# Performance work log

Measured on AMD Instinct MI355X. Metric: run time of the kernel, lower is better.

Reference implementation:

```python
import jax, jax.numpy as jnp
import numpy as np

DIM = 1024
HEADS = 16
HEAD_DIM = DIM // HEADS


def setup_inputs() -> dict:
    key = jax.random.key(0)
    ks = jax.random.split(key, 5)
    B, N = 4, 2048
    x = jax.random.normal(ks[0], (B, N, DIM), dtype=jnp.float32)
    # nn.Linear default init scale ~ 1/sqrt(fan_in)
    s = 1.0 / np.sqrt(DIM)
    W_qkv = jax.random.uniform(ks[1], (DIM, 3 * DIM), minval=-s, maxval=s, dtype=jnp.float32)
    b_qkv = jax.random.uniform(ks[2], (3 * DIM,), minval=-s, maxval=s, dtype=jnp.float32)
    W_proj = jax.random.uniform(ks[3], (DIM, DIM), minval=-s, maxval=s, dtype=jnp.float32)
    b_proj = jax.random.uniform(ks[4], (DIM,), minval=-s, maxval=s, dtype=jnp.float32)
    return {"x": x, "W_qkv": W_qkv, "b_qkv": b_qkv, "W_proj": W_proj, "b_proj": b_proj}


def reference(x, W_qkv, b_qkv, W_proj, b_proj):
    B, N, C = x.shape
    qkv = x @ W_qkv + b_qkv                      # [B, N, 3C]
    qkv = qkv.reshape(B, N, 3, HEADS, HEAD_DIM)
    q = jnp.transpose(qkv[:, :, 0], (0, 2, 1, 3))  # [B, H, N, D]
    k = jnp.transpose(qkv[:, :, 1], (0, 2, 1, 3))
    v = jnp.transpose(qkv[:, :, 2], (0, 2, 1, 3))
    scale = 1.0 / np.sqrt(HEAD_DIM)
    scores = jnp.einsum('bhqd,bhkd->bhqk', q, k) * scale  # [B, H, N, N]
    attn = jax.nn.softmax(scores, axis=-1)
    out = jnp.einsum('bhqk,bhkd->bhqd', attn, v)           # [B, H, N, D]
    out = jnp.transpose(out, (0, 2, 1, 3)).reshape(B, N, C)
    return out @ W_proj + b_proj
```

## Files before the change

kernel.cpp:

```cpp
#include <hip/hip_runtime.h>

typedef __attribute__((ext_vector_type(2)))  float  f32x2;
typedef __attribute__((ext_vector_type(4)))  float  f32x4;
typedef __attribute__((ext_vector_type(16))) float  f32x16;
typedef __attribute__((ext_vector_type(8)))  short  short8;
typedef __attribute__((ext_vector_type(4)))  unsigned int u32x4;
typedef __attribute__((ext_vector_type(2)))  unsigned int uint2v;

#define MFMA16 __builtin_amdgcn_mfma_f32_16x16x32_bf16
#define MFMA32 __builtin_amdgcn_mfma_f32_32x32x16_bf16

static __device__ __forceinline__ unsigned short f2bf(float f){
  union { float f; unsigned u; } v; v.f = f;
  unsigned r = v.u + 0x7fffu + ((v.u >> 16) & 1u);
  return (unsigned short)(r >> 16);
}

static __device__ __forceinline__ unsigned cvtpk(float a, float b){
  unsigned r;
  asm("v_cvt_pk_bf16_f32 %0, %1, %2" : "=v"(r) : "v"(a), "v"(b));
  return r;
}

static __device__ __forceinline__ void plswap(unsigned &a, unsigned &b){
  asm("v_permlane32_swap_b32 %0, %1" : "+v"(a), "+v"(b));
}

static __device__ __forceinline__ float max3f(float a, float b, float c){
  return fmaxf(fmaxf(a, b), c);
}

typedef __attribute__((address_space(1))) void gvoid_t;
typedef __attribute__((address_space(3))) void lvoid_t;

static __device__ __forceinline__ void gll16(const unsigned short* g, unsigned short* l){
  __builtin_amdgcn_global_load_lds((gvoid_t*)g, (lvoid_t*)l, 16, 0, 0);
}


__global__ __launch_bounds__(256) void k_convert(const float* __restrict__ x,
                                                 unsigned short* __restrict__ xb){
  __shared__ __align__(16) unsigned short sm[16384];
  const int mblk = blockIdx.x >> 4, kt = blockIdx.x & 15;
  const int t = threadIdx.x;
  const int l16 = t & 15, rg = t >> 4;
  #pragma unroll
  for (int p = 0; p < 16; p++){
    int row = p * 16 + rg;
    f32x4 v = *(const f32x4*)&x[(size_t)(mblk*256 + row) * 1024 + kt*64 + l16*4];
    uint2v u; u[0] = cvtpk(v[0], v[1]); u[1] = cvtpk(v[2], v[3]);
    int g = l16 >> 1;
    *(uint2v*)&sm[row*64 + ((g ^ (row & 7)) << 3) + (l16 & 1)*4] = u;
  }
  __syncthreads();
  size_t obase = (size_t)((mblk*16 + kt)*2) * 8192;
  #pragma unroll
  for (int i = 0; i < 8; i++){
    int o = i * 256 + t;
    int kh = o >> 10, rem = o & 1023;
    int band = rem >> 6, cc = (rem >> 4) & 3, ri = rem & 15;
    int r = band*16 + ri, g = kh*4 + cc;
    short8 vv = *(const short8*)&sm[r*64 + ((g ^ (r & 7)) << 3)];
    *(short8*)&xb[obase + (size_t)kh*8192 + rem*8] = vv;
  }
}

__global__ __launch_bounds__(256) void k_transpose(const float* __restrict__ W,
                                                   unsigned short* __restrict__ Wt,
                                                   int K, int N){
  __shared__ float tile[32][33];
  int n0 = blockIdx.x * 32, k0 = blockIdx.y * 32;
  int tx = threadIdx.x, ty = threadIdx.y;
  #pragma unroll
  for (int r = 0; r < 4; r++)
    tile[ty + 8*r][tx] = W[(size_t)(k0 + ty + 8*r) * N + n0 + tx];
  __syncthreads();
  #pragma unroll
  for (int r = 0; r < 4; r++){
    int nn = ty + 8*r;
    int n = n0 + nn, k = k0 + tx;
    int kt = k >> 6, kh = (k >> 5) & 1, cc = (k >> 3) & 3, ke = k & 7;
    int nblk = n >> 8, band = (n & 255) >> 4, ri = n & 15;
    Wt[(size_t)(((nblk*16 + kt)*2 + kh)) * 8192 + band*512 + cc*128 + ri*8 + ke] =
        f2bf(tile[tx][nn]);
  }
}

#define GSYNC3 { __builtin_amdgcn_sched_barrier(0);                        \
                 asm volatile("s_waitcnt vmcnt(3)" ::: "memory");          \
                 __builtin_amdgcn_s_barrier();                             \
                 __builtin_amdgcn_sched_barrier(0); }
#define GSYNC0 { __builtin_amdgcn_sched_barrier(0);                        \
                 asm volatile("s_waitcnt vmcnt(0)" ::: "memory");          \
                 __builtin_amdgcn_s_barrier();                             \
                 __builtin_amdgcn_sched_barrier(0); }

template<int MODE>
__global__ __launch_bounds__(512, 2) void k_gemm(const unsigned short* __restrict__ A,
                                                 const unsigned short* __restrict__ Bt,
                                                 const float* __restrict__ bias,
                                                 void* __restrict__ outp,
                                                 int NT){
  __shared__ __align__(16) unsigned short lds[49152];
  const int t = threadIdx.x, w = t >> 6, l = t & 63;
  const int wr = w >> 2, wc = w & 3;
  const int bx = blockIdx.x, by = blockIdx.y;
  const int mblk = bx >> 1, mhalf = bx & 1;

  const unsigned short* Ab = A + (size_t)mblk*262144 + mhalf*4096 + t*8;
  const unsigned short* Bb = Bt + (size_t)by*262144 + t*8;

  f32x4 acc[4][4];
  #pragma unroll
  for (int i = 0; i < 4; i++)
    #pragma unroll
    for (int j = 0; j < 4; j++)
      acc[i][j] = (f32x4){0.f, 0.f, 0.f, 0.f};

#define GSTAGE(c2, ks, ktile) {                                                   \
    gll16(Ab + (size_t)(ktile)*16384 + (ks)*8192, &lds[(c2)*8192 + (ks)*4096 + t*8]); \
    gll16(Bb + (size_t)(ktile)*16384 + (ks)*8192, &lds[16384 + (c2)*16384 + (ks)*8192 + t*8]); \
    gll16(Bb + (size_t)(ktile)*16384 + (ks)*8192 + 4096, &lds[16384 + (c2)*16384 + (ks)*8192 + 4096 + t*8]); }

#define GPHASE(c2, ks) {                                                          \
    short8 af[4], bfr[4];                                                         \
    const int aoff = (c2)*8192 + (ks)*4096 + wr*2048 + l*8;                       \
    const int boff = 16384 + (c2)*16384 + (ks)*8192 + wc*2048 + l*8;              \
    _Pragma("unroll")                                                             \
    for (int i = 0; i < 4; i++) af[i]  = *(const short8*)&lds[aoff + i*512];      \
    _Pragma("unroll")                                                             \
    for (int j = 0; j < 4; j++) bfr[j] = *(const short8*)&lds[boff + j*512];      \
    __builtin_amdgcn_s_setprio(1);                                                \
    _Pragma("unroll")                                                             \
    for (int i = 0; i < 4; i++)                                                   \
      _Pragma("unroll")                                                           \
      for (int j = 0; j < 4; j++)                                                 \
        acc[i][j] = MFMA16(af[i], bfr[j], acc[i][j], 0, 0, 0);                    \
    __builtin_amdgcn_s_setprio(0); }

  GSTAGE(0, 0, 0);
  GSTAGE(0, 1, 0);
  GSYNC3;

  for (int kt2 = 0; kt2 < NT; kt2++){
    const int c = kt2 & 1, n2 = c ^ 1;
    const bool pre = kt2 < NT - 1;
    if (pre) GSTAGE(n2, 0, kt2 + 1);
    GPHASE(c, 0);
    if (pre) GSYNC3 else GSYNC0;
    if (pre) GSTAGE(n2, 1, kt2 + 1);
    GPHASE(c, 1);
    if (pre) GSYNC3;
  }

  if (MODE == 0){
    unsigned short* qg = (unsigned short*)outp;
    unsigned short* kg = qg + (size_t)8388608;
    unsigned short* vg = kg + (size_t)8388608;
    const int which = by >> 2;
    const int lrow = l & 15;
    #pragma unroll
    for (int j = 0; j < 4; j++){
      int col = by*256 + wc*64 + j*16 + lrow;
      float bi = bias[col];
      int cc = col & 1023;
      int h = cc >> 6;
      int d = j*16 + lrow;
      if (which == 2){
        int db = d >> 5, dd = d & 31;
        #pragma unroll
        for (int i = 0; i < 4; i++){
          int nn = bx*128 + wr*64 + i*16 + (l >> 4)*4;
          int b = nn >> 11, key = nn & 2047;
          size_t idx = (size_t)(key >> 6)*4096 + (size_t)(((key >> 4) & 3)*2 + db)*512
                     + (((key >> 3) & 1)*32 + dd)*8 + (key & 7);
          uint2v u;
          u[0] = cvtpk(acc[i][j][0] + bi, acc[i][j][1] + bi);
          u[1] = cvtpk(acc[i][j][2] + bi, acc[i][j][3] + bi);
          *(uint2v*)&vg[(size_t)(b*16 + h)*131072 + idx] = u;
        }
      } else {
        unsigned short* dst = which ? kg : qg;
        float scale = which ? 1.0f : 0.18033688011f;
        int dsub = (d >> 4)*512 + ((d >> 3) & 1)*256 + (d & 7);
        #pragma unroll
        for (int i = 0; i < 4; i++)
          #pragma unroll
          for (int reg = 0; reg < 4; reg++){
            int nn = bx*128 + wr*64 + i*16 + (l >> 4)*4 + reg;
            int b = nn >> 11, row = nn & 2047;
            dst[(size_t)(b*16 + h)*131072 + (size_t)(row >> 5)*2048 + dsub + (row & 31)*8] =
                f2bf((acc[i][j][reg] + bi) * scale);
          }
      }
    }
  } else {
    float* out = (float*)outp;
    #pragma unroll
    for (int i = 0; i < 4; i++)
      #pragma unroll
      for (int reg = 0; reg < 4; reg++){
        int row = bx*128 + wr*64 + i*16 + (l >> 4)*4 + reg;
        #pragma unroll
        for (int j = 0; j < 4; j++){
          int col = by*256 + wc*64 + j*16 + (l & 15);
          out[(size_t)row * 1024 + col] = acc[i][j][reg] + bias[col];
        }
      }
  }
#undef GSTAGE
#undef GPHASE
}

__global__ __launch_bounds__(256, 4) void k_attn(const unsigned short* __restrict__ Qg,
                                                 const unsigned short* __restrict__ Kg,
                                                 const unsigned short* __restrict__ Vg,
                                                 unsigned short* __restrict__ aout){
  __shared__ __align__(16) unsigned short lds[20480];

  const int t = threadIdx.x, w = t >> 6, l = t & 63;
  const int hi = l >> 5, q31 = l & 31;
  const int d0 = blockIdx.x;
  const int xcd = d0 & 7, jj = d0 >> 3;
  const int bh = xcd + 8*(jj >> 4);
  const int bx = jj & 15;

  const unsigned short* Qp = Qg + (size_t)bh*131072 + (size_t)bx*8192;
  const unsigned short* Kp = Kg + (size_t)bh*131072;
  const unsigned short* Vp = Vg + (size_t)bh*131072;

  #pragma unroll
  for (int i = 0; i < 4; i++){ int c = i*256 + t; gll16(Qp + c*8, &lds[c*8]); }
  __syncthreads();
  short8 qf[4];
  #pragma unroll
  for (int ds = 0; ds < 4; ds++)
    qf[ds] = *(const short8*)&lds[(w*4 + ds)*512 + l*8];
  {
    short8 z8 = {0,0,0,0,0,0,0,0};
    *(short8*)&lds[16384 + t*16]     = z8;
    *(short8*)&lds[16384 + t*16 + 8] = z8;
  }
  __syncthreads();

  #pragma unroll
  for (int i = 0; i < 2; i++){
    int c = i*256 + t;
    gll16(Kp + c*8, &lds[c*8]);
    gll16(Vp + c*8, &lds[8192 + c*8]);
  }
  __syncthreads();

  f32x16 oacc0, oacc1;
  #pragma unroll
  for (int i = 0; i < 16; i++){ oacc0[i] = 0.f; oacc1[i] = 0.f; }
  float m = -1e30f, lsum = 0.f;
  u32x4 pfp[4];
  #pragma unroll
  for (int ks = 0; ks < 4; ks++){ pfp[ks][0]=0u; pfp[ks][1]=0u; pfp[ks][2]=0u; pfp[ks][3]=0u; }
  int s0 = 0, s1 = 1, s2 = 2;

  for (int kt = 0; kt < 32; kt++){
    const int cbk = (kt & 1) * 4096;
    if (kt < 31){
      const int nbk = cbk ^ 4096;
      const int nv  = 8192 + s1*4096;
      #pragma unroll
      for (int i = 0; i < 2; i++){
        int c = i*256 + t;
        gll16(Kp + (size_t)(kt + 1)*4096 + c*8, &lds[nbk + c*8]);
        gll16(Vp + (size_t)(kt + 1)*4096 + c*8, &lds[nv + c*8]);
      }
    }

    f32x16 sA, sB;
    #pragma unroll
    for (int i = 0; i < 16; i++){ sA[i] = 0.f; sB[i] = 0.f; }
    const int pvb = 8192 + s2*4096;
    __builtin_amdgcn_s_setprio(1);
    #pragma unroll
    for (int ds = 0; ds < 4; ds++){
      short8 kfA = *(const short8*)&lds[cbk + ds*512 + l*8];
      short8 kfB = *(const short8*)&lds[cbk + 2048 + ds*512 + l*8];
      sA = MFMA32(kfA, qf[ds], sA, 0, 0, 0);
      sB = MFMA32(kfB, qf[ds], sB, 0, 0, 0);
    }
    #pragma unroll
    for (int ks = 0; ks < 4; ks++){
      short8 pfr;
      *(u32x4*)&pfr = pfp[ks];
      short8 vf0 = *(const short8*)&lds[pvb + (ks*2 + 0)*512 + l*8];
      short8 vf1 = *(const short8*)&lds[pvb + (ks*2 + 1)*512 + l*8];
      oacc0 = MFMA32(vf0, pfr, oacc0, 0, 0, 0);
      oacc1 = MFMA32(vf1, pfr, oacc1, 0, 0, 0);
    }
    __builtin_amdgcn_s_setprio(0);

    float mx = max3f(
        max3f(max3f(sA[0], sA[1], sA[2]),  max3f(sA[3], sA[4], sA[5]),
              max3f(sA[6], sA[7], sA[8])),
        max3f(max3f(sA[9], sA[10], sA[11]), max3f(sA[12], sA[13], sA[14]),
              max3f(sA[15], sB[0], sB[1])),
        max3f(max3f(max3f(sB[2], sB[3], sB[4]),  max3f(sB[5], sB[6], sB[7]),
                    max3f(sB[8], sB[9], sB[10])),
              max3f(sB[11], sB[12], sB[13]),
              fmaxf(sB[14], sB[15])));
    mx = fmaxf(mx, __shfl_xor(mx, 32));
    if (!__all(mx - m <= 8.0f)){
      float mn = fmaxf(m, mx);
      float sf = __builtin_amdgcn_exp2f(m - mn);
      m = mn; lsum *= sf;
      #pragma unroll
      for (int i = 0; i < 16; i++){ oacc0[i] *= sf; oacc1[i] *= sf; }
    }
    f32x2 mm; mm[0] = m; mm[1] = m;
    f32x2 a2[8], b2[8];
    #pragma unroll
    for (int j = 0; j < 8; j++){
      f32x2 ta; ta[0] = sA[2*j]; ta[1] = sA[2*j+1];
      f32x2 tb; tb[0] = sB[2*j]; tb[1] = sB[2*j+1];
      a2[j] = ta - mm;
      b2[j] = tb - mm;
    }
    #pragma unroll
    for (int j = 0; j < 8; j++){
      a2[j][0] = __builtin_amdgcn_exp2f(a2[j][0]);
      a2[j][1] = __builtin_amdgcn_exp2f(a2[j][1]);
      b2[j][0] = __builtin_amdgcn_exp2f(b2[j][0]);
      b2[j][1] = __builtin_amdgcn_exp2f(b2[j][1]);
    }
    f32x2 s2v = ((a2[0] + a2[1]) + (a2[2] + a2[3])) + ((a2[4] + a2[5]) + (a2[6] + a2[7]))
              + ((b2[0] + b2[1]) + (b2[2] + b2[3])) + ((b2[4] + b2[5]) + (b2[6] + b2[7]));
    float rs = s2v[0] + s2v[1];
    rs += __shfl_xor(rs, 32);
    lsum += rs;

    unsigned wA[8], wB[8];
    #pragma unroll
    for (int j = 0; j < 8; j++){
      wA[j] = cvtpk(a2[j][0], a2[j][1]);
      wB[j] = cvtpk(b2[j][0], b2[j][1]);
    }
    { unsigned a = wA[0], b = wA[2]; plswap(a, b); pfp[0][0] = a; pfp[0][2] = b; }
    { unsigned a = wA[1], b = wA[3]; plswap(a, b); pfp[0][1] = a; pfp[0][3] = b; }
    { unsigned a = wA[4], b = wA[6]; plswap(a, b); pfp[1][0] = a; pfp[1][2] = b; }
    { unsigned a = wA[5], b = wA[7]; plswap(a, b); pfp[1][1] = a; pfp[1][3] = b; }
    { unsigned a = wB[0], b = wB[2]; plswap(a, b); pfp[2][0] = a; pfp[2][2] = b; }
    { unsigned a = wB[1], b = wB[3]; plswap(a, b); pfp[2][1] = a; pfp[2][3] = b; }
    { unsigned a = wB[4], b = wB[6]; plswap(a, b); pfp[3][0] = a; pfp[3][2] = b; }
    { unsigned a = wB[5], b = wB[7]; plswap(a, b); pfp[3][1] = a; pfp[3][3] = b; }

    __syncthreads();
    int tmp = s2; s2 = s0; s0 = s1; s1 = tmp;
  }

  {
    const int pvb = 8192 + s2*4096;
    __builtin_amdgcn_s_setprio(1);
    #pragma unroll
    for (int ks = 0; ks < 4; ks++){
      short8 pfr;
      *(u32x4*)&pfr = pfp[ks];
      short8 vf0 = *(const short8*)&lds[pvb + (ks*2 + 0)*512 + l*8];
      short8 vf1 = *(const short8*)&lds[pvb + (ks*2 + 1)*512 + l*8];
      oacc0 = MFMA32(vf0, pfr, oacc0, 0, 0, 0);
      oacc1 = MFMA32(vf1, pfr, oacc1, 0, 0, 0);
    }
    __builtin_amdgcn_s_setprio(0);
  }

  {
    float inv = 1.0f / lsum;
    int qrow = w*32 + q31;
    #pragma unroll
    for (int j = 0; j < 8; j++){
      int dd0 = 8*(j >> 1) + 2*(j & 1) + 4*hi;
      unsigned u0 = cvtpk(oacc0[2*j] * inv, oacc0[2*j+1] * inv);
      *(unsigned*)&lds[qrow*64 + (((dd0 >> 3) ^ (qrow & 7)) << 3) + (dd0 & 7)] = u0;
      int dd1 = dd0 + 32;
      unsigned u1 = cvtpk(oacc1[2*j] * inv, oacc1[2*j+1] * inv);
      *(unsigned*)&lds[qrow*64 + (((dd1 >> 3) ^ (qrow & 7)) << 3) + (dd1 & 7)] = u1;
    }
  }
  __syncthreads();
  {
    int mblk16 = (bh >> 4)*8 + (bx >> 1);
    int h = bh & 15;
    int bandbase = 8*(bx & 1);
    #pragma unroll
    for (int i = 0; i < 4; i++){
      int idx = i*256 + t;
      int kh = idx >> 9, band_l = (idx >> 6) & 7, cc = (idx >> 4) & 3, ri = idx & 15;
      int r = band_l*16 + ri, g = kh*4 + cc;
      short8 vv = *(const short8*)&lds[r*64 + ((g ^ (r & 7)) << 3)];
      size_t chunk = (size_t)((mblk16*16 + h)*2 + kh);
      *(short8*)&aout[chunk*8192 + (size_t)(bandbase + band_l)*512 + cc*128 + ri*8] = vv;
    }
  }
}

extern "C" void kernel_launch(void* const* d_in, const int* in_sizes, int n_in,
                              void* d_out, int out_size, void* d_ws, size_t ws_size,
                              hipStream_t stream){
  const float* x     = (const float*)d_in[0];
  const float* Wqkv  = (const float*)d_in[1];
  const float* bqkv  = (const float*)d_in[2];
  const float* Wproj = (const float*)d_in[3];
  const float* bproj = (const float*)d_in[4];

  unsigned short* ws   = (unsigned short*)d_ws;
  unsigned short* xb   = ws;
  unsigned short* Wqt  = ws + (size_t)8192 * 1024;
  unsigned short* Wpt  = Wqt + (size_t)3072 * 1024;
  unsigned short* qkvb = Wpt + (size_t)1024 * 1024;

  k_convert<<<512, 256, 0, stream>>>(x, xb);
  k_transpose<<<dim3(96, 32), dim3(32, 8), 0, stream>>>(Wqkv, Wqt, 1024, 3072);
  k_transpose<<<dim3(32, 32), dim3(32, 8), 0, stream>>>(Wproj, Wpt, 1024, 1024);
  k_gemm<0><<<dim3(64, 12), 512, 0, stream>>>(xb, Wqt, bqkv, qkvb, 16);
  k_attn<<<1024, 256, 0, stream>>>(qkvb, qkvb + (size_t)8388608,
                                   qkvb + (size_t)16777216, xb);
  k_gemm<1><<<dim3(64, 4), 512, 0, stream>>>(xb, Wpt, bproj, (void*)d_out, 16);
}
```

Baseline: 188.2 us.

## Deepen GEMM LDS pipeline to four slots with three loads in flight

Rewrites the k_gemm main loop from a double-buffered two-phase scheme into a four-slot ring of half-k-tile stages with three stages prefetched ahead. Each phase reads its LDS fragments, issues the next global-to-LDS load, then uses a single barrier before the MFMAs. The aim is to hide more global memory latency and drop one barrier per phase, using the same 48K-short LDS footprint. The risk is that correctness now depends on tight vmcnt accounting and a single barrier guarding slot reuse.

```diff
diff --git a/kernel.cpp b/kernel.cpp
--- a/kernel.cpp
+++ b/kernel.cpp
@@ -86,12 +86,8 @@
   }
 }
 
-#define GSYNC3 { __builtin_amdgcn_sched_barrier(0);                        \
-                 asm volatile("s_waitcnt vmcnt(3)" ::: "memory");          \
-                 __builtin_amdgcn_s_barrier();                             \
-                 __builtin_amdgcn_sched_barrier(0); }
-#define GSYNC0 { __builtin_amdgcn_sched_barrier(0);                        \
-                 asm volatile("s_waitcnt vmcnt(0)" ::: "memory");          \
+#define VMW(N) { __builtin_amdgcn_sched_barrier(0);                        \
+                 asm volatile("s_waitcnt vmcnt(" #N ")" ::: "memory");     \
                  __builtin_amdgcn_s_barrier();                             \
                  __builtin_amdgcn_sched_barrier(0); }
 
@@ -117,41 +113,46 @@
     for (int j = 0; j < 4; j++)
       acc[i][j] = (f32x4){0.f, 0.f, 0.f, 0.f};
 
-#define GSTAGE(c2, ks, ktile) {                                                   \
-    gll16(Ab + (size_t)(ktile)*16384 + (ks)*8192, &lds[(c2)*8192 + (ks)*4096 + t*8]); \
-    gll16(Bb + (size_t)(ktile)*16384 + (ks)*8192, &lds[16384 + (c2)*16384 + (ks)*8192 + t*8]); \
-    gll16(Bb + (size_t)(ktile)*16384 + (ks)*8192 + 4096, &lds[16384 + (c2)*16384 + (ks)*8192 + 4096 + t*8]); }
-
-#define GPHASE(c2, ks) {                                                          \
-    short8 af[4], bfr[4];                                                         \
-    const int aoff = (c2)*8192 + (ks)*4096 + wr*2048 + l*8;                       \
-    const int boff = 16384 + (c2)*16384 + (ks)*8192 + wc*2048 + l*8;              \
-    _Pragma("unroll")                                                             \
-    for (int i = 0; i < 4; i++) af[i]  = *(const short8*)&lds[aoff + i*512];      \
-    _Pragma("unroll")                                                             \
-    for (int j = 0; j < 4; j++) bfr[j] = *(const short8*)&lds[boff + j*512];      \
-    __builtin_amdgcn_s_setprio(1);                                                \
-    _Pragma("unroll")                                                             \
-    for (int i = 0; i < 4; i++)                                                   \
-      _Pragma("unroll")                                                           \
-      for (int j = 0; j < 4; j++)                                                 \
-        acc[i][j] = MFMA16(af[i], bfr[j], acc[i][j], 0, 0, 0);                    \
-    __builtin_amdgcn_s_setprio(0); }
-
-  GSTAGE(0, 0, 0);
-  GSTAGE(0, 1, 0);
-  GSYNC3;
-
-  for (int kt2 = 0; kt2 < NT; kt2++){
-    const int c = kt2 & 1, n2 = c ^ 1;
-    const bool pre = kt2 < NT - 1;
-    if (pre) GSTAGE(n2, 0, kt2 + 1);
-    GPHASE(c, 0);
-    if (pre) GSYNC3 else GSYNC0;
-    if (pre) GSTAGE(n2, 1, kt2 + 1);
-    GPHASE(c, 1);
-    if (pre) GSYNC3;
-  }
+  auto stage = [&](int sl){
+    const int b = sl & 3;
+    const size_t off = (size_t)sl * 8192;
+    gll16(Ab + off,        &lds[b*12288 + t*8]);
+    gll16(Bb + off,        &lds[b*12288 + 4096 + t*8]);
+    gll16(Bb + off + 4096, &lds[b*12288 + 8192 + t*8]);
+  };
+
+  auto phase = [&](int b, bool do_stage, int sl){
+    short8 af[4], bfr[4];
+    const int aoff = b*12288 + wr*2048 + l*8;
+    const int boff = b*12288 + 4096 + wc*2048 + l*8;
+    #pragma unroll
+    for (int i = 0; i < 4; i++) af[i]  = *(const short8*)&lds[aoff + i*512];
+    #pragma unroll
+    for (int j = 0; j < 4; j++) bfr[j] = *(const short8*)&lds[boff + j*512];
+    if (do_stage) stage(sl);
+    __builtin_amdgcn_sched_barrier(0);
+    __builtin_amdgcn_s_barrier();
+    __builtin_amdgcn_s_setprio(1);
+    #pragma unroll
+    for (int i = 0; i < 4; i++)
+      #pragma unroll
+      for (int j = 0; j < 4; j++)
+        acc[i][j] = MFMA16(af[i], bfr[j], acc[i][j], 0, 0, 0);
+    __builtin_amdgcn_s_setprio(0);
+  };
+
+  stage(0); stage(1); stage(2);
+  VMW(6);
+
+  const int NP = 2 * NT;
+  int p = 0;
+  for (; p <= NP - 4; ++p){
+    phase(p & 3, true, p + 3);
+    VMW(6);
+  }
+  phase(p & 3, false, 0); VMW(3); ++p;
+  phase(p & 3, false, 0); VMW(0); ++p;
+  phase(p & 3, false, 0);
 
   if (MODE == 0){
     unsigned short* qg = (unsigned short*)outp;
@@ -208,8 +209,6 @@
         }
       }
   }
-#undef GSTAGE
-#undef GPHASE
 }
 
 __global__ __launch_bounds__(256, 4) void k_attn(const unsigned short* __restrict__ Qg,
```

New measurement: 182.9 us. 1.03x faster.
